# Kernel tuning notes

Hardware: AMD Instinct MI355X
Metric: run time of the kernel (lower is better)

The kernel has to match this reference:

```python
import jax, jax.numpy as jnp
import numpy as np

A = 10      # number of areas of interest
NPA = 192   # neurons per area
C = 128     # n_channels_per_region
B, T = 32, 1024
N = A * NPA # 1920 total neurons


def setup_inputs() -> dict:
    key = jax.random.key(0)
    k1, k2, k3 = jax.random.split(key, 3)
    x = jax.random.normal(k1, (B, T, N), jnp.float32)
    # per-area linear weights, stored [A, n_in, n_out] (nn.Linear W.T), and biases
    W = jax.random.normal(k2, (A, NPA, C), jnp.float32) / np.sqrt(NPA)
    b = jax.random.normal(k3, (A, C), jnp.float32) * 0.01
    # area label per neuron, identical across batch (code uses neuron_regions[0]);
    # permute neuron order so the per-area gather is irregular
    labels = jnp.repeat(jnp.arange(A, dtype=jnp.int32), NPA)
    perm = jax.random.permutation(jax.random.key(7), N)
    labels = labels[perm]
    neuron_regions = jnp.tile(labels[None, :], (B, 1))
    is_left = jnp.zeros((B, N), dtype=bool)  # unused by forward body
    return {"x": x, "W": W, "b": b, "neuron_regions": neuron_regions, "is_left": is_left}


def reference(x, W, b, neuron_regions, is_left):
    # halfbin_X=0, smoothing=False -> preprocess_X is identity, repeat_interleave no-op
    nr = np.asarray(neuron_regions[0])                      # static per-session labels
    A_, n, C_ = W.shape
    # gather indices per area; equal counts per area -> rectangular [A, n]
    idx = np.stack([np.where(nr == a)[0] for a in range(A_)])
    x_area = x[:, :, idx]                                   # [B, T, A, n] gather
    emb = jnp.einsum('btan,anc->btac', x_area, W) + b       # per-area small linear
    Bq, Tq = x.shape[0], x.shape[1]
    # scatter: area a writes channels [a*C, (a+1)*C) -> contiguous reshape
    return emb.reshape(Bq, Tq, A_ * C_)
```

## Files before the change

kernel.cpp:

```cpp
#include <hip/hip_runtime.h>
#include <stdint.h>

#define A_    10
#define NPA_  192
#define C_    128
#define N_    1920
#define M_    32768
#define OUTC  1280
#define MT    16
#define RS    1928

typedef __attribute__((ext_vector_type(8))) short  short8;
typedef __attribute__((ext_vector_type(4))) float  float4v;

__device__ __forceinline__ unsigned short f2bf(float f) {
  unsigned u = __builtin_bit_cast(unsigned, f);
  u += 0x7FFFu + ((u >> 16) & 1u);
  return (unsigned short)(u >> 16);
}

__global__ __launch_bounds__(256) void prep_kernel(const float* __restrict__ W,
                                                   const int* __restrict__ nr,
                                                   unsigned short* __restrict__ Wt,
                                                   int* __restrict__ dest) {
  if (blockIdx.x == 0) {
    int lane = threadIdx.x;
    if (lane < 64) {
      int cnt[A_];
#pragma unroll
      for (int i = 0; i < A_; ++i) cnt[i] = 0;
      unsigned long long lt = (1ull << lane) - 1ull;
      for (int ch = 0; ch < N_ / 64; ++ch) {
        int p = ch * 64 + lane;
        int a = nr[p];
        int base = 0, rank = 0;
#pragma unroll
        for (int aa = 0; aa < A_; ++aa) {
          unsigned long long m = __ballot(a == aa);
          if (a == aa) { base = cnt[aa]; rank = __popcll(m & lt); }
          cnt[aa] += __popcll(m);
        }
        dest[p] = a * NPA_ + base + rank;
      }
    }
  } else {
    int o  = (blockIdx.x - 1) * 256 + threadIdx.x;
    int ac = o / NPA_;
    int k  = o - ac * NPA_;
    int a  = ac >> 7;
    int c  = ac & 127;
    Wt[o] = f2bf(W[(a * NPA_ + k) * C_ + c]);
  }
}

__global__ __launch_bounds__(256, 2) void stitch_kernel(const float* __restrict__ x,
                                                        const unsigned short* __restrict__ Wt,
                                                        const float* __restrict__ bias,
                                                        const int* __restrict__ dest,
                                                        float* __restrict__ out) {
  __shared__ unsigned short xs[MT * RS];

  const int tid = threadIdx.x;
  const int mb  = blockIdx.x * MT;

  const float4* xp = (const float4*)(x + (size_t)mb * N_);
  const int4*   dp = (const int4*)dest;
#pragma unroll
  for (int i = 0; i < 30; ++i) {
    int g   = i * 256 + tid;
    int row = g / 480;
    int c4  = g - row * 480;
    float4 v = xp[g];
    int4   d = dp[c4];
    unsigned short* base = xs + row * RS;
    base[d.x] = f2bf(v.x);
    base[d.y] = f2bf(v.y);
    base[d.z] = f2bf(v.z);
    base[d.w] = f2bf(v.w);
  }
  __syncthreads();

  const int wave = tid >> 6;
  const int lane = tid & 63;
  const int l15  = lane & 15;
  const int lq   = lane >> 4;

  short8 af[6];
  int    cur_a = -1;
  const int t0 = wave * 20;

  short8 bf[6];
  {
    int t = t0, a = t >> 3, cc = t & 7;
    const short8* wp = (const short8*)(Wt + (size_t)(a * C_ + cc * 16 + l15) * NPA_);
#pragma unroll
    for (int ks = 0; ks < 6; ++ks) bf[ks] = wp[ks * 4 + lq];
  }

  for (int t = t0; t < t0 + 20; ++t) {
    int a = t >> 3, cc = t & 7;
    if (a != cur_a) {
#pragma unroll
      for (int ks = 0; ks < 6; ++ks)
        af[ks] = *(const short8*)&xs[l15 * RS + a * NPA_ + ks * 32 + lq * 8];
      cur_a = a;
    }
    float bv = bias[a * C_ + cc * 16 + l15];

    short8 bfn[6];
    if (t + 1 < t0 + 20) {
      int t2 = t + 1, a2 = t2 >> 3, cc2 = t2 & 7;
      const short8* wp2 = (const short8*)(Wt + (size_t)(a2 * C_ + cc2 * 16 + l15) * NPA_);
#pragma unroll
      for (int ks = 0; ks < 6; ++ks) bfn[ks] = wp2[ks * 4 + lq];
    }

    float4v acc = {0.f, 0.f, 0.f, 0.f};
#pragma unroll
    for (int ks = 0; ks < 6; ++ks)
      acc = __builtin_amdgcn_mfma_f32_16x16x32_bf16(af[ks], bf[ks], acc, 0, 0, 0);

    float* op = out + (size_t)(mb + lq * 4) * OUTC + a * C_ + cc * 16 + l15;
#pragma unroll
    for (int r = 0; r < 4; ++r) op[(size_t)r * OUTC] = acc[r] + bv;

#pragma unroll
    for (int ks = 0; ks < 6; ++ks) bf[ks] = bfn[ks];
  }
}

extern "C" void kernel_launch(void* const* d_in, const int* in_sizes, int n_in,
                              void* d_out, int out_size, void* d_ws, size_t ws_size,
                              hipStream_t stream) {
  const float* x    = (const float*)d_in[0];
  const float* W    = (const float*)d_in[1];
  const float* b    = (const float*)d_in[2];
  const int*   nr   = (const int*)  d_in[3];
  float*       out  = (float*)d_out;

  unsigned short* Wt   = (unsigned short*)d_ws;
  int*            dest = (int*)((char*)d_ws + 491520);

  prep_kernel<<<dim3(961), dim3(256), 0, stream>>>(W, nr, Wt, dest);
  stitch_kernel<<<dim3(M_ / MT), dim3(256), 0, stream>>>(x, Wt, b, dest, out);
}
```

Baseline: 497.7 us.

## Halve row tile, narrow dest indices to u16, batch gather loads for occupancy

Cuts the rows per block from 16 to 8, which halves LDS use so up to 5 blocks can share a CU (launch bounds raised to match). The scatter-destination table becomes 16-bit, and x loads are issued in batches before the LDS scatter to overlap memory latency. The MFMA now duplicates the 8 real rows into both halves of its 16-row A operand, and only half the lanes store results. This wastes half of each MFMA and re-reads the W fragments per block, twice as many times overall, in exchange for more parallelism.

```diff
diff --git a/kernel.cpp b/kernel.cpp
--- a/kernel.cpp
+++ b/kernel.cpp
@@ -7,7 +7,7 @@
 #define N_    1920
 #define M_    32768
 #define OUTC  1280
-#define MT    16
+#define MT    8
 #define RS    1928
 
 typedef __attribute__((ext_vector_type(8))) short  short8;
@@ -22,7 +22,7 @@
 __global__ __launch_bounds__(256) void prep_kernel(const float* __restrict__ W,
                                                    const int* __restrict__ nr,
                                                    unsigned short* __restrict__ Wt,
-                                                   int* __restrict__ dest) {
+                                                   unsigned short* __restrict__ dest) {
   if (blockIdx.x == 0) {
     int lane = threadIdx.x;
     if (lane < 64) {
@@ -40,7 +40,7 @@
           if (a == aa) { base = cnt[aa]; rank = __popcll(m & lt); }
           cnt[aa] += __popcll(m);
         }
-        dest[p] = a * NPA_ + base + rank;
+        dest[p] = (unsigned short)(a * NPA_ + base + rank);
       }
     }
   } else {
@@ -53,10 +53,10 @@
   }
 }
 
-__global__ __launch_bounds__(256, 2) void stitch_kernel(const float* __restrict__ x,
+__global__ __launch_bounds__(256, 5) void stitch_kernel(const float* __restrict__ x,
                                                         const unsigned short* __restrict__ Wt,
                                                         const float* __restrict__ bias,
-                                                        const int* __restrict__ dest,
+                                                        const unsigned short* __restrict__ dest,
                                                         float* __restrict__ out) {
   __shared__ unsigned short xs[MT * RS];
 
@@ -64,19 +64,45 @@
   const int mb  = blockIdx.x * MT;
 
   const float4* xp = (const float4*)(x + (size_t)mb * N_);
-  const int4*   dp = (const int4*)dest;
+  {
+    float4 v[8]; ushort4 dd[8];
 #pragma unroll
-  for (int i = 0; i < 30; ++i) {
-    int g   = i * 256 + tid;
-    int row = g / 480;
-    int c4  = g - row * 480;
-    float4 v = xp[g];
-    int4   d = dp[c4];
-    unsigned short* base = xs + row * RS;
-    base[d.x] = f2bf(v.x);
-    base[d.y] = f2bf(v.y);
-    base[d.z] = f2bf(v.z);
-    base[d.w] = f2bf(v.w);
+    for (int i = 0; i < 8; ++i) {
+      int g = i * 256 + tid;
+      int row = g / 480, c4 = g - row * 480;
+      v[i]  = xp[g];
+      dd[i] = *(const ushort4*)(dest + 4 * c4);
+    }
+#pragma unroll
+    for (int i = 0; i < 8; ++i) {
+      int g = i * 256 + tid;
+      int row = g / 480;
+      unsigned short* basep = xs + row * RS;
+      basep[dd[i].x] = f2bf(v[i].x);
+      basep[dd[i].y] = f2bf(v[i].y);
+      basep[dd[i].z] = f2bf(v[i].z);
+      basep[dd[i].w] = f2bf(v[i].w);
+    }
+  }
+  {
+    float4 v[7]; ushort4 dd[7];
+#pragma unroll
+    for (int i = 0; i < 7; ++i) {
+      int g = (i + 8) * 256 + tid;
+      int row = g / 480, c4 = g - row * 480;
+      v[i]  = xp[g];
+      dd[i] = *(const ushort4*)(dest + 4 * c4);
+    }
+#pragma unroll
+    for (int i = 0; i < 7; ++i) {
+      int g = (i + 8) * 256 + tid;
+      int row = g / 480;
+      unsigned short* basep = xs + row * RS;
+      basep[dd[i].x] = f2bf(v[i].x);
+      basep[dd[i].y] = f2bf(v[i].y);
+      basep[dd[i].z] = f2bf(v[i].z);
+      basep[dd[i].w] = f2bf(v[i].w);
+    }
   }
   __syncthreads();
 
@@ -84,6 +110,7 @@
   const int lane = tid & 63;
   const int l15  = lane & 15;
   const int lq   = lane >> 4;
+  const int arow = (l15 & 7);
 
   short8 af[6];
   int    cur_a = -1;
@@ -102,7 +129,7 @@
     if (a != cur_a) {
 #pragma unroll
       for (int ks = 0; ks < 6; ++ks)
-        af[ks] = *(const short8*)&xs[l15 * RS + a * NPA_ + ks * 32 + lq * 8];
+        af[ks] = *(const short8*)&xs[arow * RS + a * NPA_ + ks * 32 + lq * 8];
       cur_a = a;
     }
     float bv = bias[a * C_ + cc * 16 + l15];
@@ -120,9 +147,11 @@
     for (int ks = 0; ks < 6; ++ks)
       acc = __builtin_amdgcn_mfma_f32_16x16x32_bf16(af[ks], bf[ks], acc, 0, 0, 0);
 
-    float* op = out + (size_t)(mb + lq * 4) * OUTC + a * C_ + cc * 16 + l15;
+    if (lq < 2) {
+      float* op = out + (size_t)(mb + lq * 4) * OUTC + a * C_ + cc * 16 + l15;
 #pragma unroll
-    for (int r = 0; r < 4; ++r) op[(size_t)r * OUTC] = acc[r] + bv;
+      for (int r = 0; r < 4; ++r) op[(size_t)r * OUTC] = acc[r] + bv;
+    }
 
 #pragma unroll
     for (int ks = 0; ks < 6; ++ks) bf[ks] = bfn[ks];
@@ -139,7 +168,7 @@
   float*       out  = (float*)d_out;
 
   unsigned short* Wt   = (unsigned short*)d_ws;
-  int*            dest = (int*)((char*)d_ws + 491520);
+  unsigned short* dest = (unsigned short*)((char*)d_ws + 491520);
 
   prep_kernel<<<dim3(961), dim3(256), 0, stream>>>(W, nr, Wt, dest);
   stitch_kernel<<<dim3(M_ / MT), dim3(256), 0, stream>>>(x, Wt, b, dest, out);
```

After: 576.7 us. +15.9%, slower.
